# Kernel tuning notes

Measured on AMD Instinct MI355X. Metric: run time of the kernel, lower is better.

## Reference

```python
import jax, jax.numpy as jnp
import numpy as np

# config dims (see shape_source)
NO = 8        # Max_Object
NT = 32       # Max_Time
C = 512       # feat_dims
VD = 1024     # visual_dim
RD = 300      # self.nfeat (relation word-vector dim)
H = 4         # headnum
B = 8         # batch
No = NT * 2 * NO      # 512 object-graph nodes
Nr = NT * NO * NO     # 2048 relation-graph nodes


def _glorot(key, shape):
    fan_in = shape[0]
    return jax.random.normal(key, shape, dtype=jnp.float32) / np.sqrt(fan_in)


def setup_inputs() -> dict:
    key = jax.random.key(0)
    ks = jax.random.split(key, 18)
    inp = {
        "Ao": jax.random.uniform(ks[0], (B, No, No), dtype=jnp.float32),
        "srco": jax.random.normal(ks[1], (B, 1, 1, No, VD), dtype=jnp.float32),
        "Ar": jax.random.uniform(ks[2], (B, Nr, Nr), dtype=jnp.float32),
        "srcr": jax.random.normal(ks[3], (B, 1, 1, Nr, RD), dtype=jnp.float32),
        # GraphConvolution weights: gcl_o/gcl2_o and gcl_r/gcl2_r
        "Wo1": _glorot(ks[4], (VD, 1024)),
        "Wo2": _glorot(ks[5], (1024, C)),
        "Wr1": _glorot(ks[6], (RD, 1024)),
        "Wr2": _glorot(ks[7], (1024, C)),
        # MultiHeadAttention (e2n) projections
        "Wq": _glorot(ks[8], (C, C)), "bq": jnp.zeros((C,), jnp.float32),
        "Wk": _glorot(ks[9], (C, C)), "bk": jnp.zeros((C,), jnp.float32),
        "Wv": _glorot(ks[10], (C, C)), "bv": jnp.zeros((C,), jnp.float32),
        "Wp": _glorot(ks[11], (C, C)), "bp": jnp.zeros((C,), jnp.float32),
        # e2n_embed: Linear(2C -> C)
        "We": _glorot(ks[12], (2 * C, C)), "be": jnp.zeros((C,), jnp.float32),
    }
    return inp


def _gcn2(A, x, W1, W2):
    """Two stacked GraphConvolution layers with self-loops: relu((A+I) @ x @ W).
    A: (b,N,N), x: (b,N,Din). Vectorized over batch (torch code loops per-sample)."""
    eye = jnp.eye(A.shape[-1], dtype=A.dtype)
    Ah = A + eye
    h = jax.nn.relu(jnp.einsum('bij,bjd->bid', Ah, x @ W1))
    return jax.nn.relu(jnp.einsum('bij,bjd->bid', Ah, h @ W2))


def _mha(x, Wq, bq, Wk, bk, Wv, bv, Wp, bp):
    """Standard multi-head self-attention. x: (Bseg, S, C)."""
    Bs, S, _ = x.shape
    dh = C // H
    q = (x @ Wq + bq).reshape(Bs, S, H, dh)
    k = (x @ Wk + bk).reshape(Bs, S, H, dh)
    v = (x @ Wv + bv).reshape(Bs, S, H, dh)
    attn = jax.nn.softmax(jnp.einsum('bqhd,bkhd->bhqk', q, k) / np.sqrt(dh), axis=-1)
    o = jnp.einsum('bhqk,bkhd->bqhd', attn, v).reshape(Bs, S, C)
    return o @ Wp + bp


def _forward(Ao, srco, Ar, srcr, Wo1, Wo2, Wr1, Wr2,
             Wq, bq, Wk, bk, Wv, bv, Wp, bp, We, be):
    b = Ao.shape[0]
    # object-graph GCN (torch loops over batch; vectorized here)
    xo = srco[:, 0, 0, :, :VD]                       # (b, No, VD)
    srco_gcn = _gcn2(Ao, xo, Wo1, Wo2)               # (b, No, C)
    out_gcn_o = srco_gcn.reshape(b, NT, 2 * NO, C)
    # relation-graph GCN
    xr = srcr[:, 0, 0]                               # (b, Nr, RD)
    srcr_gcn = _gcn2(Ar, xr, Wr1, Wr2)               # (b, Nr, C)
    out_gcn_r = srcr_gcn.reshape(b, NT, NO * NO, C)
    # compute_e2n: segment-wise MHA over NO-token windows (torch loops over NO)
    r = out_gcn_r.reshape(b * NT, NO, NO, C)
    seg_a = r.reshape(b * NT * NO, NO, C)                      # rows of NOxNO grid
    a = _mha(seg_a, Wq, bq, Wk, bk, Wv, bv, Wp, bp).mean(axis=1)
    a = a.reshape(b * NT, NO, C)
    seg_o = jnp.swapaxes(r, 1, 2).reshape(b * NT * NO, NO, C)  # cols (permute 0,2,1,3)
    o = _mha(seg_o, Wq, bq, Wk, bk, Wv, bv, Wp, bp).mean(axis=1)
    o = o.reshape(b * NT, NO, C)
    tmp = jnp.concatenate([a, o], axis=1)                      # (b*NT, 2*NO, C)
    cat = jnp.concatenate([tmp, out_gcn_o.reshape(b * NT, 2 * NO, C)], axis=-1)
    out_e2n = cat @ We + be
    return out_e2n.reshape(b, NT, 2 * NO, C)


def reference(Ao, srco, Ar, srcr, Wo1, Wo2, Wr1, Wr2,
              Wq, bq, Wk, bk, Wv, bv, Wp, bp, We, be):
    return _forward(Ao, srco, Ar, srcr, Wo1, Wo2, Wr1, Wr2,
                    Wq, bq, Wk, bk, Wv, bv, Wp, bp, We, be)
```

## Files before the change

kernel.cpp:

```cpp
#include <hip/hip_runtime.h>
#include <hip/hip_bf16.h>


typedef __attribute__((ext_vector_type(4))) float f32x4;
typedef __attribute__((ext_vector_type(8))) short bf16x8s;

#define TILE 128
#define BKK 32
#define LDSS 40

__device__ inline void split2(float a, float b, unsigned& h, unsigned& l) {
    __hip_bfloat16 ha = __float2bfloat16(a), hb = __float2bfloat16(b);
    float ra = __bfloat162float(ha), rb = __bfloat162float(hb);
    __hip_bfloat16 la = __float2bfloat16(a - ra), lb = __float2bfloat16(b - rb);
    unsigned short uha = *(unsigned short*)&ha, uhb = *(unsigned short*)&hb;
    unsigned short ula = *(unsigned short*)&la, ulb = *(unsigned short*)&lb;
    h = (unsigned)uha | ((unsigned)uhb << 16);
    l = (unsigned)ula | ((unsigned)ulb << 16);
}

__global__ __launch_bounds__(256) void gemm_split2(
    const float* __restrict__ A, long long sA, int lda,
    const float* __restrict__ BT, long long sBT, int ldbt,
    float* __restrict__ D, long long sD, int ldd,
    const float* __restrict__ addN, long long sAddN, int ldaddN,
    const float* __restrict__ addT, long long sAddT, int ldaddT,
    const float* __restrict__ bias,
    int K, int relu)
{
    __shared__ __hip_bfloat16 Ah[TILE * LDSS], Al[TILE * LDSS];
    __shared__ __hip_bfloat16 Bh[TILE * LDSS], Bl[TILE * LDSS];

    const int tid  = threadIdx.x;
    const int lane = tid & 63;
    const int wave = tid >> 6;
    const int wm   = (wave >> 1) * 64;
    const int wn   = (wave & 1) * 64;
    const int row0 = blockIdx.y * TILE;
    const int col0 = blockIdx.x * TILE;
    const int b    = blockIdx.z;

    const float* Ab = A  + (size_t)b * sA;
    const float* Bb = BT + (size_t)b * sBT;

    f32x4 acc[4][4];
#pragma unroll
    for (int i = 0; i < 4; ++i)
#pragma unroll
        for (int j = 0; j < 4; ++j) acc[i][j] = (f32x4){0.f, 0.f, 0.f, 0.f};

    const int quad = lane >> 4;
    const int l16  = lane & 15;

    for (int k0 = 0; k0 < K; k0 += BKK) {
        __syncthreads();
#pragma unroll
        for (int it = 0; it < 2; ++it) {
            int task = tid + it * 256;
            int m = task >> 2, kq = task & 3;
            const float* ap = Ab + (size_t)(row0 + m) * lda + k0 + kq * 8;
            float4 v0 = *(const float4*)ap;
            float4 v1 = *(const float4*)(ap + 4);
            uint4 H, L;
            split2(v0.x, v0.y, H.x, L.x); split2(v0.z, v0.w, H.y, L.y);
            split2(v1.x, v1.y, H.z, L.z); split2(v1.z, v1.w, H.w, L.w);
            *(uint4*)(&Ah[m * LDSS + kq * 8]) = H;
            *(uint4*)(&Al[m * LDSS + kq * 8]) = L;
        }
#pragma unroll
        for (int it = 0; it < 2; ++it) {
            int task = tid + it * 256;
            int n = task >> 2, kq = task & 3;
            const float* bp = Bb + (size_t)(col0 + n) * ldbt + k0 + kq * 8;
            float4 v0 = *(const float4*)bp;
            float4 v1 = *(const float4*)(bp + 4);
            uint4 H, L;
            split2(v0.x, v0.y, H.x, L.x); split2(v0.z, v0.w, H.y, L.y);
            split2(v1.x, v1.y, H.z, L.z); split2(v1.z, v1.w, H.w, L.w);
            *(uint4*)(&Bh[n * LDSS + kq * 8]) = H;
            *(uint4*)(&Bl[n * LDSS + kq * 8]) = L;
        }
        __syncthreads();

        bf16x8s ah[4], al[4], bh[4], bl[4];
#pragma unroll
        for (int mt = 0; mt < 4; ++mt) {
            int r = (wm + mt * 16 + l16) * LDSS + quad * 8;
            ah[mt] = *(const bf16x8s*)(&Ah[r]);
            al[mt] = *(const bf16x8s*)(&Al[r]);
        }
#pragma unroll
        for (int nt = 0; nt < 4; ++nt) {
            int r = (wn + nt * 16 + l16) * LDSS + quad * 8;
            bh[nt] = *(const bf16x8s*)(&Bh[r]);
            bl[nt] = *(const bf16x8s*)(&Bl[r]);
        }
#pragma unroll
        for (int mt = 0; mt < 4; ++mt)
#pragma unroll
            for (int nt = 0; nt < 4; ++nt) {
                acc[mt][nt] = __builtin_amdgcn_mfma_f32_16x16x32_bf16(ah[mt], bh[nt], acc[mt][nt], 0, 0, 0);
                acc[mt][nt] = __builtin_amdgcn_mfma_f32_16x16x32_bf16(ah[mt], bl[nt], acc[mt][nt], 0, 0, 0);
                acc[mt][nt] = __builtin_amdgcn_mfma_f32_16x16x32_bf16(al[mt], bh[nt], acc[mt][nt], 0, 0, 0);
            }
    }

    float* Db = D + (size_t)b * sD;
    const float* AddN = addN ? addN + (size_t)b * sAddN : nullptr;
    const float* AddT = addT ? addT + (size_t)b * sAddT : nullptr;
#pragma unroll
    for (int mt = 0; mt < 4; ++mt)
#pragma unroll
        for (int nt = 0; nt < 4; ++nt)
#pragma unroll
            for (int r = 0; r < 4; ++r) {
                int m = row0 + wm + mt * 16 + quad * 4 + r;
                int n = col0 + wn + nt * 16 + l16;
                float v = acc[mt][nt][r];
                if (AddN) v += AddN[(size_t)m * ldaddN + n];
                if (AddT) v += AddT[(size_t)n * ldaddT + m];
                if (bias) v += bias[n];
                if (relu && v < 0.f) v = 0.f;
                Db[(size_t)m * ldd + n] = v;
            }
}

__global__ __launch_bounds__(256) void padtrans(
    const float* __restrict__ src, float* __restrict__ dst,
    int R, int C, int Rp, int Cp)
{
    __shared__ float T[64][65];
    const int t = threadIdx.x;
    const int tr = t >> 4, tc = t & 15;
    const int c0 = blockIdx.x * 64, r0 = blockIdx.y * 64;
    const size_t bat = blockIdx.z;
    const float* sb = src + bat * (size_t)R * C;
    float* db = dst + bat * (size_t)Cp * Rp;

#pragma unroll
    for (int i = 0; i < 4; ++i) {
        int rr = tr + i * 16;
        int gr = r0 + rr;
        float v0 = 0.f, v1 = 0.f, v2 = 0.f, v3 = 0.f;
        if (gr < R) {
            int c = c0 + tc * 4;
            const float* s = sb + (size_t)gr * C + c;
            if (c + 0 < C) v0 = s[0];
            if (c + 1 < C) v1 = s[1];
            if (c + 2 < C) v2 = s[2];
            if (c + 3 < C) v3 = s[3];
        }
        T[rr][tc * 4 + 0] = v0; T[rr][tc * 4 + 1] = v1;
        T[rr][tc * 4 + 2] = v2; T[rr][tc * 4 + 3] = v3;
    }
    __syncthreads();
#pragma unroll
    for (int i = 0; i < 4; ++i) {
        int cc = tr + i * 16;
        float4 v = { T[tc * 4 + 0][cc], T[tc * 4 + 1][cc],
                     T[tc * 4 + 2][cc], T[tc * 4 + 3][cc] };
        *(float4*)(db + (size_t)(c0 + cc) * Rp + r0 + tc * 4) = v;
    }
}

__global__ __launch_bounds__(256) void gemm_bf16(
    const __hip_bfloat16* __restrict__ A, long long sA, int lda,
    const __hip_bfloat16* __restrict__ B, long long sB, int ldb,
    void* __restrict__ D, long long sD, int ldd,
    const __hip_bfloat16* __restrict__ addsrc, long long sAdd, int ldadd,
    const float* __restrict__ bias,
    int K, int relu, int outF32)
{
    __shared__ __hip_bfloat16 As[TILE * LDSS];
    __shared__ __hip_bfloat16 Bs[TILE * LDSS];

    const int tid  = threadIdx.x;
    const int lane = tid & 63;
    const int wave = tid >> 6;
    const int wm   = (wave >> 1) * 64;
    const int wn   = (wave & 1) * 64;
    const int row0 = blockIdx.y * TILE;
    const int col0 = blockIdx.x * TILE;
    const int b    = blockIdx.z;

    const __hip_bfloat16* Ab = A + (size_t)b * sA;
    const __hip_bfloat16* Bb = B + (size_t)b * sB;

    f32x4 acc[4][4];
#pragma unroll
    for (int i = 0; i < 4; ++i)
#pragma unroll
        for (int j = 0; j < 4; ++j) acc[i][j] = (f32x4){0.f, 0.f, 0.f, 0.f};

    const int quad = lane >> 4;
    const int l16  = lane & 15;

    for (int k0 = 0; k0 < K; k0 += BKK) {
        __syncthreads();
#pragma unroll
        for (int it = 0; it < 2; ++it) {
            int task = tid + it * 256;
            int m = task >> 2, kq = task & 3;
            uint4 val = *(const uint4*)(Ab + (size_t)(row0 + m) * lda + k0 + kq * 8);
            *(uint4*)(&As[m * LDSS + kq * 8]) = val;
        }
#pragma unroll
        for (int it = 0; it < 2; ++it) {
            int task = tid + it * 256;
            int kk = task >> 4, n8 = task & 15;
            uint4 val = *(const uint4*)(Bb + (size_t)(k0 + kk) * ldb + col0 + n8 * 8);
            const __hip_bfloat16* v16 = (const __hip_bfloat16*)&val;
#pragma unroll
            for (int u = 0; u < 8; ++u)
                Bs[(n8 * 8 + u) * LDSS + kk] = v16[u];
        }
        __syncthreads();

        bf16x8s afrag[4], bfrag[4];
#pragma unroll
        for (int mt = 0; mt < 4; ++mt)
            afrag[mt] = *(const bf16x8s*)(&As[(wm + mt * 16 + l16) * LDSS + quad * 8]);
#pragma unroll
        for (int nt = 0; nt < 4; ++nt)
            bfrag[nt] = *(const bf16x8s*)(&Bs[(wn + nt * 16 + l16) * LDSS + quad * 8]);
#pragma unroll
        for (int mt = 0; mt < 4; ++mt)
#pragma unroll
            for (int nt = 0; nt < 4; ++nt)
                acc[mt][nt] = __builtin_amdgcn_mfma_f32_16x16x32_bf16(
                    afrag[mt], bfrag[nt], acc[mt][nt], 0, 0, 0);
    }

    __hip_bfloat16* Db16 = (__hip_bfloat16*)D + (size_t)b * sD;
    float*          DbF  = (float*)D + (size_t)b * sD;
    const __hip_bfloat16* Addb = addsrc ? addsrc + (size_t)b * sAdd : nullptr;
#pragma unroll
    for (int mt = 0; mt < 4; ++mt)
#pragma unroll
        for (int nt = 0; nt < 4; ++nt)
#pragma unroll
            for (int r = 0; r < 4; ++r) {
                int m = row0 + wm + mt * 16 + quad * 4 + r;
                int n = col0 + wn + nt * 16 + l16;
                float v = acc[mt][nt][r];
                if (Addb) v += __bfloat162float(Addb[(size_t)m * ldadd + n]);
                if (bias) v += bias[n];
                if (relu && v < 0.f) v = 0.f;
                if (outF32) DbF[(size_t)m * ldd + n] = v;
                else        Db16[(size_t)m * ldd + n] = __float2bfloat16(v);
            }
}

__global__ void convert_kernel(const float* __restrict__ src,
                               __hip_bfloat16* __restrict__ dst, int n4)
{
    int i = blockIdx.x * blockDim.x + threadIdx.x;
    if (i >= n4) return;
    float4 v = ((const float4*)src)[i];
    __hip_bfloat16 t0 = __float2bfloat16(v.x), t1 = __float2bfloat16(v.y);
    __hip_bfloat16 t2 = __float2bfloat16(v.z), t3 = __float2bfloat16(v.w);
    ushort4 o = { *(unsigned short*)&t0, *(unsigned short*)&t1,
                  *(unsigned short*)&t2, *(unsigned short*)&t3 };
    ((ushort4*)dst)[i] = o;
}

__global__ __launch_bounds__(256) void attn_kernel(
    const float* __restrict__ q,
    const float* __restrict__ k,
    const float* __restrict__ v,
    __hip_bfloat16* __restrict__ abar)
{
    __shared__ float qs[8][512], ks[8][512], vs[8][512];
    __shared__ float sc[4][8][8];
    __shared__ float wb[4][8];

    const int tid  = threadIdx.x;
    const int mode = blockIdx.y;
    const int g    = blockIdx.x >> 3;
    const int idx  = blockIdx.x & 7;
    const int rowBase = g * 64;

    for (int t = tid; t < 512; t += 256) {
        int p = t >> 6, c8 = (t & 63) * 8;
        int row = (mode == 0) ? (rowBase + idx * 8 + p) : (rowBase + p * 8 + idx);
        const float* qp = q + (size_t)row * 512 + c8;
        const float* kp = k + (size_t)row * 512 + c8;
        const float* vp = v + (size_t)row * 512 + c8;
        *(float4*)(&qs[p][c8])     = *(const float4*)(qp);
        *(float4*)(&qs[p][c8 + 4]) = *(const float4*)(qp + 4);
        *(float4*)(&ks[p][c8])     = *(const float4*)(kp);
        *(float4*)(&ks[p][c8 + 4]) = *(const float4*)(kp + 4);
        *(float4*)(&vs[p][c8])     = *(const float4*)(vp);
        *(float4*)(&vs[p][c8 + 4]) = *(const float4*)(vp + 4);
    }
    __syncthreads();

    {
        int h = tid >> 6, l = tid & 63;
        int i = l >> 3, j = l & 7;
        const float* qrow = &qs[i][h * 128];
        const float* krow = &ks[j][h * 128];
        float s = 0.f;
#pragma unroll
        for (int d = 0; d < 128; d += 4) {
            float4 qa = *(const float4*)(qrow + d);
            float4 kb = *(const float4*)(krow + d);
            s += qa.x * kb.x + qa.y * kb.y + qa.z * kb.z + qa.w * kb.w;
        }
        sc[h][i][j] = s * 0.08838834764831845f;
    }
    __syncthreads();

    if (tid < 32) {
        int h = tid >> 3, i = tid & 7;
        float mx = -1e30f;
#pragma unroll
        for (int j = 0; j < 8; ++j) mx = fmaxf(mx, sc[h][i][j]);
        float e[8], sum = 0.f;
#pragma unroll
        for (int j = 0; j < 8; ++j) { e[j] = __expf(sc[h][i][j] - mx); sum += e[j]; }
        float inv = 1.f / sum;
#pragma unroll
        for (int j = 0; j < 8; ++j) sc[h][i][j] = e[j] * inv;
    }
    __syncthreads();

    if (tid < 32) {
        int h = tid >> 3, j = tid & 7;
        float s = 0.f;
#pragma unroll
        for (int i = 0; i < 8; ++i) s += sc[h][i][j];
        wb[h][j] = s * 0.125f;
    }
    __syncthreads();

    {
        int orow = g * 16 + mode * 8 + idx;
        for (int c = tid; c < 512; c += 256) {
            int h = c >> 7;
            float o = 0.f;
#pragma unroll
            for (int j = 0; j < 8; ++j) o += wb[h][j] * vs[j][c];
            abar[(size_t)orow * 512 + c] = __float2bfloat16(o);
        }
    }
}


extern "C" void kernel_launch(void* const* d_in, const int* in_sizes, int n_in,
                              void* d_out, int out_size, void* d_ws, size_t ws_size,
                              hipStream_t stream)
{
    const float* Ao   = (const float*)d_in[0];
    const float* srco = (const float*)d_in[1];
    const float* Ar   = (const float*)d_in[2];
    const float* srcr = (const float*)d_in[3];
    const float* Wo1  = (const float*)d_in[4];
    const float* Wo2  = (const float*)d_in[5];
    const float* Wr1  = (const float*)d_in[6];
    const float* Wr2  = (const float*)d_in[7];
    const float* Wq   = (const float*)d_in[8];
    const float* bq   = (const float*)d_in[9];
    const float* Wk   = (const float*)d_in[10];
    const float* bk   = (const float*)d_in[11];
    const float* Wv   = (const float*)d_in[12];
    const float* bv   = (const float*)d_in[13];
    const float* Wp   = (const float*)d_in[14];
    const float* bp   = (const float*)d_in[15];
    const float* We   = (const float*)d_in[16];
    const float* be   = (const float*)d_in[17];
    float* out = (float*)d_out;

    char* ws = (char*)d_ws;
    const size_t R0 = 0;
    const size_t R1 = 67108864;
    const size_t R2 = 100663296;
    const size_t R3 = 134217728;
    const size_t R4 = 167772160;
    const size_t R5 = 192937984;

    float* HRf  = (float*)(ws + R0);
    float* qF   = (float*)(ws + R0);
    float* kF   = (float*)(ws + R0 + 33554432);
    float* T2Rf = (float*)(ws + R1);
    float* vF   = (float*)(ws + R1);
    float* Uf   = (float*)(ws + R2);
    float* T2RT = (float*)(ws + R2);
    float* GRf  = (float*)(ws + R3);
    float* XPT  = (float*)(ws + R4);
    __hip_bfloat16* ABAR = (__hip_bfloat16*)(ws + R4);
    float* WPT  = (float*)(ws + R5);
    float* Wr2T = (float*)(ws + R5 + 1310720);
    float* WqT  = (float*)(ws + R5 + 3407872);
    float* WkT  = (float*)(ws + R5 + 4456448);
    float* WvT  = (float*)(ws + R5 + 5505024);

    __hip_bfloat16* TO    = (__hip_bfloat16*)(ws + R2 + 0);
    __hip_bfloat16* HO    = (__hip_bfloat16*)(ws + R2 + 8388608);
    __hip_bfloat16* T2O   = (__hip_bfloat16*)(ws + R2 + 16777216);
    __hip_bfloat16* CAT   = (__hip_bfloat16*)(ws + R2 + 20971520);
    __hip_bfloat16* srcoB = (__hip_bfloat16*)(ws + R2 + 29360128);
    __hip_bfloat16* AoB   = (__hip_bfloat16*)(ws + R2 + 37748736);
    __hip_bfloat16* Wo1B  = (__hip_bfloat16*)(ws + R2 + 41943040);
    __hip_bfloat16* Wo2B  = (__hip_bfloat16*)(ws + R2 + 44040192);
    __hip_bfloat16* WeB   = (__hip_bfloat16*)(ws + R2 + 45088768);
    __hip_bfloat16* WpB   = (__hip_bfloat16*)(ws + R2 + 46137344);

    dim3 blk(256);
    auto cvt = [&](const float* s, __hip_bfloat16* d, int n) {
        convert_kernel<<<dim3((n / 4 + 255) / 256), blk, 0, stream>>>(s, d, n / 4);
    };

    padtrans<<<dim3(6, 32, 8), blk, 0, stream>>>(srcr, XPT, 2048, 300, 2048, 384);
    padtrans<<<dim3(16, 5, 1), blk, 0, stream>>>(Wr1, WPT, 300, 1024, 320, 1024);
    padtrans<<<dim3(8, 16, 1), blk, 0, stream>>>(Wr2, Wr2T, 1024, 512, 1024, 512);
    padtrans<<<dim3(8, 8, 1), blk, 0, stream>>>(Wq, WqT, 512, 512, 512, 512);
    padtrans<<<dim3(8, 8, 1), blk, 0, stream>>>(Wk, WkT, 512, 512, 512, 512);
    padtrans<<<dim3(8, 8, 1), blk, 0, stream>>>(Wv, WvT, 512, 512, 512, 512);

    gemm_split2<<<dim3(3, 16, 8), blk, 0, stream>>>(
        Ar, 2048LL * 2048, 2048, XPT, 384LL * 2048, 2048,
        Uf, 2048LL * 384, 384, nullptr, 0, 0, XPT, 384LL * 2048, 2048,
        nullptr, 2048, 0);
    gemm_split2<<<dim3(8, 128, 1), blk, 0, stream>>>(
        Uf, 0, 384, WPT, 0, 320,
        HRf, 0, 1024, nullptr, 0, 0, nullptr, 0, 0,
        nullptr, 320, 1);
    gemm_split2<<<dim3(4, 128, 1), blk, 0, stream>>>(
        HRf, 0, 1024, Wr2T, 0, 1024,
        T2Rf, 0, 512, nullptr, 0, 0, nullptr, 0, 0,
        nullptr, 1024, 0);
    padtrans<<<dim3(8, 32, 8), blk, 0, stream>>>(T2Rf, T2RT, 2048, 512, 2048, 512);
    gemm_split2<<<dim3(4, 16, 8), blk, 0, stream>>>(
        Ar, 2048LL * 2048, 2048, T2RT, 512LL * 2048, 2048,
        GRf, 2048LL * 512, 512, T2Rf, 2048LL * 512, 512, nullptr, 0, 0,
        nullptr, 2048, 1);
    gemm_split2<<<dim3(4, 128, 1), blk, 0, stream>>>(
        GRf, 0, 512, WqT, 0, 512, qF, 0, 512,
        nullptr, 0, 0, nullptr, 0, 0, bq, 512, 0);
    gemm_split2<<<dim3(4, 128, 1), blk, 0, stream>>>(
        GRf, 0, 512, WkT, 0, 512, kF, 0, 512,
        nullptr, 0, 0, nullptr, 0, 0, bk, 512, 0);
    gemm_split2<<<dim3(4, 128, 1), blk, 0, stream>>>(
        GRf, 0, 512, WvT, 0, 512, vF, 0, 512,
        nullptr, 0, 0, nullptr, 0, 0, bv, 512, 0);
    attn_kernel<<<dim3(2048, 2), blk, 0, stream>>>(qF, kF, vF, ABAR);

    cvt(srco, srcoB, 4194304);
    cvt(Ao, AoB, 2097152);
    cvt(Wo1, Wo1B, 1048576);
    cvt(Wo2, Wo2B, 524288);
    cvt(We, WeB, 524288);
    cvt(Wp, WpB, 262144);
    gemm_bf16<<<dim3(8, 32, 1), blk, 0, stream>>>(srcoB, 0, 1024, Wo1B, 0, 1024,
        TO, 0, 1024, nullptr, 0, 0, nullptr, 1024, 0, 0);
    gemm_bf16<<<dim3(8, 4, 8), blk, 0, stream>>>(AoB, 512LL * 512, 512, TO, 512LL * 1024, 1024,
        HO, 512LL * 1024, 1024, TO, 512LL * 1024, 1024, nullptr, 512, 1, 0);
    gemm_bf16<<<dim3(4, 32, 1), blk, 0, stream>>>(HO, 0, 1024, Wo2B, 0, 512,
        T2O, 0, 512, nullptr, 0, 0, nullptr, 1024, 0, 0);
    gemm_bf16<<<dim3(4, 4, 8), blk, 0, stream>>>(AoB, 512LL * 512, 512, T2O, 512LL * 512, 512,
        (void*)(CAT + 512), 512LL * 1024, 1024, T2O, 512LL * 512, 512, nullptr, 512, 1, 0);
    gemm_bf16<<<dim3(4, 32, 1), blk, 0, stream>>>(ABAR, 0, 512, WpB, 0, 512,
        CAT, 0, 1024, nullptr, 0, 0, bp, 512, 0, 0);
    gemm_bf16<<<dim3(4, 32, 1), blk, 0, stream>>>(CAT, 0, 1024, WeB, 0, 512,
        out, 0, 512, nullptr, 0, 0, be, 1024, 0, 1);
}
```

Before: 1.200 ms.

## Store intermediates as pre-split bf16 hi/lo planes instead of fp32

The split-bf16 GEMM pipeline now writes its intermediates and transposed weights directly as bf16 high/low planes, so the following GEMMs load them without doing a per-tile fp32-to-bf16 split. This removes repeated split arithmetic inside the GEMM main loops. It also keeps global traffic roughly the same, since two bf16 planes take the same bytes as one fp32. Only the large Ar operand is still split on the fly. Each producer epilogue now does scalar 2-byte stores to two planes, which may be less efficient than before.

```diff
diff --git a/kernel.cpp b/kernel.cpp
--- a/kernel.cpp
+++ b/kernel.cpp
@@ -19,13 +19,22 @@
     l = (unsigned)ula | ((unsigned)ulb << 16);
 }
 
-__global__ __launch_bounds__(256) void gemm_split2(
+__device__ inline void splitw(float v, unsigned short& h, unsigned short& l) {
+    __hip_bfloat16 hb = __float2bfloat16(v);
+    __hip_bfloat16 lb = __float2bfloat16(v - __bfloat162float(hb));
+    h = *(unsigned short*)&hb;
+    l = *(unsigned short*)&lb;
+}
+
+__global__ __launch_bounds__(256) void gemm_asplit(
     const float* __restrict__ A, long long sA, int lda,
-    const float* __restrict__ BT, long long sBT, int ldbt,
-    float* __restrict__ D, long long sD, int ldd,
+    const __hip_bfloat16* __restrict__ BTh, const __hip_bfloat16* __restrict__ BTl,
+    long long sBT, int ldbt,
+    __hip_bfloat16* __restrict__ Dh_, __hip_bfloat16* __restrict__ Dl_,
+    long long sD, int ldd,
     const float* __restrict__ addN, long long sAddN, int ldaddN,
-    const float* __restrict__ addT, long long sAddT, int ldaddT,
-    const float* __restrict__ bias,
+    const __hip_bfloat16* __restrict__ addTh, const __hip_bfloat16* __restrict__ addTl,
+    long long sAddT, int ldaddT,
     int K, int relu)
 {
     __shared__ __hip_bfloat16 Ah[TILE * LDSS], Al[TILE * LDSS];
@@ -40,8 +49,9 @@
     const int col0 = blockIdx.x * TILE;
     const int b    = blockIdx.z;
 
-    const float* Ab = A  + (size_t)b * sA;
-    const float* Bb = BT + (size_t)b * sBT;
+    const float* Ab = A + (size_t)b * sA;
+    const __hip_bfloat16* Bbh = BTh + (size_t)b * sBT;
+    const __hip_bfloat16* Bbl = BTl + (size_t)b * sBT;
 
     f32x4 acc[4][4];
 #pragma unroll
@@ -71,14 +81,9 @@
         for (int it = 0; it < 2; ++it) {
             int task = tid + it * 256;
             int n = task >> 2, kq = task & 3;
-            const float* bp = Bb + (size_t)(col0 + n) * ldbt + k0 + kq * 8;
-            float4 v0 = *(const float4*)bp;
-            float4 v1 = *(const float4*)(bp + 4);
-            uint4 H, L;
-            split2(v0.x, v0.y, H.x, L.x); split2(v0.z, v0.w, H.y, L.y);
-            split2(v1.x, v1.y, H.z, L.z); split2(v1.z, v1.w, H.w, L.w);
-            *(uint4*)(&Bh[n * LDSS + kq * 8]) = H;
-            *(uint4*)(&Bl[n * LDSS + kq * 8]) = L;
+            size_t off = (size_t)(col0 + n) * ldbt + k0 + kq * 8;
+            *(uint4*)(&Bh[n * LDSS + kq * 8]) = *(const uint4*)(Bbh + off);
+            *(uint4*)(&Bl[n * LDSS + kq * 8]) = *(const uint4*)(Bbl + off);
         }
         __syncthreads();
 
@@ -105,9 +110,11 @@
             }
     }
 
-    float* Db = D + (size_t)b * sD;
+    __hip_bfloat16* Dhb = Dh_ + (size_t)b * sD;
+    __hip_bfloat16* Dlb = Dl_ + (size_t)b * sD;
     const float* AddN = addN ? addN + (size_t)b * sAddN : nullptr;
-    const float* AddT = addT ? addT + (size_t)b * sAddT : nullptr;
+    const __hip_bfloat16* ATh = addTh ? addTh + (size_t)b * sAddT : nullptr;
+    const __hip_bfloat16* ATl = addTl ? addTl + (size_t)b * sAddT : nullptr;
 #pragma unroll
     for (int mt = 0; mt < 4; ++mt)
 #pragma unroll
@@ -118,15 +125,124 @@
                 int n = col0 + wn + nt * 16 + l16;
                 float v = acc[mt][nt][r];
                 if (AddN) v += AddN[(size_t)m * ldaddN + n];
-                if (AddT) v += AddT[(size_t)n * ldaddT + m];
+                if (ATh) v += __bfloat162float(ATh[(size_t)n * ldaddT + m])
+                            + __bfloat162float(ATl[(size_t)n * ldaddT + m]);
+                if (relu && v < 0.f) v = 0.f;
+                unsigned short hh, ll;
+                splitw(v, hh, ll);
+                size_t o = (size_t)m * ldd + n;
+                *(unsigned short*)&Dhb[o] = hh;
+                *(unsigned short*)&Dlb[o] = ll;
+            }
+}
+
+__global__ __launch_bounds__(256) void gemm_planes(
+    const __hip_bfloat16* __restrict__ Aph, const __hip_bfloat16* __restrict__ Apl,
+    long long sA, int lda,
+    const __hip_bfloat16* __restrict__ BTh, const __hip_bfloat16* __restrict__ BTl,
+    long long sBT, int ldbt,
+    void* __restrict__ D, __hip_bfloat16* __restrict__ Dl_, long long sD, int ldd,
+    const float* __restrict__ bias,
+    int K, int relu, int outMode)
+{
+    __shared__ __hip_bfloat16 Ah[TILE * LDSS], Al[TILE * LDSS];
+    __shared__ __hip_bfloat16 Bh[TILE * LDSS], Bl[TILE * LDSS];
+
+    const int tid  = threadIdx.x;
+    const int lane = tid & 63;
+    const int wave = tid >> 6;
+    const int wm   = (wave >> 1) * 64;
+    const int wn   = (wave & 1) * 64;
+    const int row0 = blockIdx.y * TILE;
+    const int col0 = blockIdx.x * TILE;
+    const int b    = blockIdx.z;
+
+    const __hip_bfloat16* Abh = Aph + (size_t)b * sA;
+    const __hip_bfloat16* Abl = Apl + (size_t)b * sA;
+    const __hip_bfloat16* Bbh = BTh + (size_t)b * sBT;
+    const __hip_bfloat16* Bbl = BTl + (size_t)b * sBT;
+
+    f32x4 acc[4][4];
+#pragma unroll
+    for (int i = 0; i < 4; ++i)
+#pragma unroll
+        for (int j = 0; j < 4; ++j) acc[i][j] = (f32x4){0.f, 0.f, 0.f, 0.f};
+
+    const int quad = lane >> 4;
+    const int l16  = lane & 15;
+
+    for (int k0 = 0; k0 < K; k0 += BKK) {
+        __syncthreads();
+#pragma unroll
+        for (int it = 0; it < 2; ++it) {
+            int task = tid + it * 256;
+            int m = task >> 2, kq = task & 3;
+            size_t off = (size_t)(row0 + m) * lda + k0 + kq * 8;
+            *(uint4*)(&Ah[m * LDSS + kq * 8]) = *(const uint4*)(Abh + off);
+            *(uint4*)(&Al[m * LDSS + kq * 8]) = *(const uint4*)(Abl + off);
+        }
+#pragma unroll
+        for (int it = 0; it < 2; ++it) {
+            int task = tid + it * 256;
+            int n = task >> 2, kq = task & 3;
+            size_t off = (size_t)(col0 + n) * ldbt + k0 + kq * 8;
+            *(uint4*)(&Bh[n * LDSS + kq * 8]) = *(const uint4*)(Bbh + off);
+            *(uint4*)(&Bl[n * LDSS + kq * 8]) = *(const uint4*)(Bbl + off);
+        }
+        __syncthreads();
+
+        bf16x8s ah[4], al[4], bh[4], bl[4];
+#pragma unroll
+        for (int mt = 0; mt < 4; ++mt) {
+            int r = (wm + mt * 16 + l16) * LDSS + quad * 8;
+            ah[mt] = *(const bf16x8s*)(&Ah[r]);
+            al[mt] = *(const bf16x8s*)(&Al[r]);
+        }
+#pragma unroll
+        for (int nt = 0; nt < 4; ++nt) {
+            int r = (wn + nt * 16 + l16) * LDSS + quad * 8;
+            bh[nt] = *(const bf16x8s*)(&Bh[r]);
+            bl[nt] = *(const bf16x8s*)(&Bl[r]);
+        }
+#pragma unroll
+        for (int mt = 0; mt < 4; ++mt)
+#pragma unroll
+            for (int nt = 0; nt < 4; ++nt) {
+                acc[mt][nt] = __builtin_amdgcn_mfma_f32_16x16x32_bf16(ah[mt], bh[nt], acc[mt][nt], 0, 0, 0);
+                acc[mt][nt] = __builtin_amdgcn_mfma_f32_16x16x32_bf16(ah[mt], bl[nt], acc[mt][nt], 0, 0, 0);
+                acc[mt][nt] = __builtin_amdgcn_mfma_f32_16x16x32_bf16(al[mt], bh[nt], acc[mt][nt], 0, 0, 0);
+            }
+    }
+
+    float* DbF = (float*)D + (size_t)b * sD;
+    __hip_bfloat16* Dhb = (__hip_bfloat16*)D + (size_t)b * sD;
+    __hip_bfloat16* Dlb = Dl_ ? Dl_ + (size_t)b * sD : nullptr;
+#pragma unroll
+    for (int mt = 0; mt < 4; ++mt)
+#pragma unroll
+        for (int nt = 0; nt < 4; ++nt)
+#pragma unroll
+            for (int r = 0; r < 4; ++r) {
+                int m = row0 + wm + mt * 16 + quad * 4 + r;
+                int n = col0 + wn + nt * 16 + l16;
+                float v = acc[mt][nt][r];
                 if (bias) v += bias[n];
                 if (relu && v < 0.f) v = 0.f;
-                Db[(size_t)m * ldd + n] = v;
+                if (outMode == 0) {
+                    DbF[(size_t)m * ldd + n] = v;
+                } else {
+                    unsigned short hh, ll;
+                    splitw(v, hh, ll);
+                    size_t o = (size_t)m * ldd + n;
+                    *(unsigned short*)&Dhb[o] = hh;
+                    *(unsigned short*)&Dlb[o] = ll;
+                }
             }
 }
 
-__global__ __launch_bounds__(256) void padtrans(
-    const float* __restrict__ src, float* __restrict__ dst,
+__global__ __launch_bounds__(256) void padtrans_split(
+    const float* __restrict__ src,
+    __hip_bfloat16* __restrict__ dsth, __hip_bfloat16* __restrict__ dstl,
     int R, int C, int Rp, int Cp)
 {
     __shared__ float T[64][65];
@@ -135,7 +251,8 @@
     const int c0 = blockIdx.x * 64, r0 = blockIdx.y * 64;
     const size_t bat = blockIdx.z;
     const float* sb = src + bat * (size_t)R * C;
-    float* db = dst + bat * (size_t)Cp * Rp;
+    __hip_bfloat16* dhb = dsth + bat * (size_t)Cp * Rp;
+    __hip_bfloat16* dlb = dstl + bat * (size_t)Cp * Rp;
 
 #pragma unroll
     for (int i = 0; i < 4; ++i) {
@@ -159,7 +276,12 @@
         int cc = tr + i * 16;
         float4 v = { T[tc * 4 + 0][cc], T[tc * 4 + 1][cc],
                      T[tc * 4 + 2][cc], T[tc * 4 + 3][cc] };
-        *(float4*)(db + (size_t)(c0 + cc) * Rp + r0 + tc * 4) = v;
+        ushort4 H, L;
+        splitw(v.x, H.x, L.x); splitw(v.y, H.y, L.y);
+        splitw(v.z, H.z, L.z); splitw(v.w, H.w, L.w);
+        size_t off = (size_t)(c0 + cc) * Rp + r0 + tc * 4;
+        *(ushort4*)(dhb + off) = H;
+        *(ushort4*)(dlb + off) = L;
     }
 }
 
@@ -379,21 +501,31 @@
     const size_t R4 = 167772160;
     const size_t R5 = 192937984;
 
-    float* HRf  = (float*)(ws + R0);
+    __hip_bfloat16* HRh = (__hip_bfloat16*)(ws + R0);
+    __hip_bfloat16* HRl = HRh + 16777216;
     float* qF   = (float*)(ws + R0);
     float* kF   = (float*)(ws + R0 + 33554432);
     float* T2Rf = (float*)(ws + R1);
     float* vF   = (float*)(ws + R1);
-    float* Uf   = (float*)(ws + R2);
-    float* T2RT = (float*)(ws + R2);
-    float* GRf  = (float*)(ws + R3);
-    float* XPT  = (float*)(ws + R4);
+    __hip_bfloat16* Uh = (__hip_bfloat16*)(ws + R2);
+    __hip_bfloat16* Ul = Uh + 6291456;
+    __hip_bfloat16* T2RTh = (__hip_bfloat16*)(ws + R2);
+    __hip_bfloat16* T2RTl = T2RTh + 8388608;
+    __hip_bfloat16* GRh = (__hip_bfloat16*)(ws + R3);
+    __hip_bfloat16* GRl = GRh + 8388608;
+    __hip_bfloat16* XPTh = (__hip_bfloat16*)(ws + R4);
+    __hip_bfloat16* XPTl = XPTh + 6291456;
     __hip_bfloat16* ABAR = (__hip_bfloat16*)(ws + R4);
-    float* WPT  = (float*)(ws + R5);
-    float* Wr2T = (float*)(ws + R5 + 1310720);
-    float* WqT  = (float*)(ws + R5 + 3407872);
-    float* WkT  = (float*)(ws + R5 + 4456448);
-    float* WvT  = (float*)(ws + R5 + 5505024);
+    __hip_bfloat16* WPTh = (__hip_bfloat16*)(ws + R5);
+    __hip_bfloat16* WPTl = WPTh + 327680;
+    __hip_bfloat16* Wr2Th = (__hip_bfloat16*)(ws + R5 + 1310720);
+    __hip_bfloat16* Wr2Tl = Wr2Th + 524288;
+    __hip_bfloat16* WqTh = (__hip_bfloat16*)(ws + R5 + 3407872);
+    __hip_bfloat16* WqTl = WqTh + 262144;
+    __hip_bfloat16* WkTh = (__hip_bfloat16*)(ws + R5 + 4456448);
+    __hip_bfloat16* WkTl = WkTh + 262144;
+    __hip_bfloat16* WvTh = (__hip_bfloat16*)(ws + R5 + 5505024);
+    __hip_bfloat16* WvTl = WvTh + 262144;
 
     __hip_bfloat16* TO    = (__hip_bfloat16*)(ws + R2 + 0);
     __hip_bfloat16* HO    = (__hip_bfloat16*)(ws + R2 + 8388608);
@@ -411,39 +543,39 @@
         convert_kernel<<<dim3((n / 4 + 255) / 256), blk, 0, stream>>>(s, d, n / 4);
     };
 
-    padtrans<<<dim3(6, 32, 8), blk, 0, stream>>>(srcr, XPT, 2048, 300, 2048, 384);
-    padtrans<<<dim3(16, 5, 1), blk, 0, stream>>>(Wr1, WPT, 300, 1024, 320, 1024);
-    padtrans<<<dim3(8, 16, 1), blk, 0, stream>>>(Wr2, Wr2T, 1024, 512, 1024, 512);
-    padtrans<<<dim3(8, 8, 1), blk, 0, stream>>>(Wq, WqT, 512, 512, 512, 512);
-    padtrans<<<dim3(8, 8, 1), blk, 0, stream>>>(Wk, WkT, 512, 512, 512, 512);
-    padtrans<<<dim3(8, 8, 1), blk, 0, stream>>>(Wv, WvT, 512, 512, 512, 512);
-
-    gemm_split2<<<dim3(3, 16, 8), blk, 0, stream>>>(
-        Ar, 2048LL * 2048, 2048, XPT, 384LL * 2048, 2048,
-        Uf, 2048LL * 384, 384, nullptr, 0, 0, XPT, 384LL * 2048, 2048,
-        nullptr, 2048, 0);
-    gemm_split2<<<dim3(8, 128, 1), blk, 0, stream>>>(
-        Uf, 0, 384, WPT, 0, 320,
-        HRf, 0, 1024, nullptr, 0, 0, nullptr, 0, 0,
-        nullptr, 320, 1);
-    gemm_split2<<<dim3(4, 128, 1), blk, 0, stream>>>(
-        HRf, 0, 1024, Wr2T, 0, 1024,
-        T2Rf, 0, 512, nullptr, 0, 0, nullptr, 0, 0,
-        nullptr, 1024, 0);
-    padtrans<<<dim3(8, 32, 8), blk, 0, stream>>>(T2Rf, T2RT, 2048, 512, 2048, 512);
-    gemm_split2<<<dim3(4, 16, 8), blk, 0, stream>>>(
-        Ar, 2048LL * 2048, 2048, T2RT, 512LL * 2048, 2048,
-        GRf, 2048LL * 512, 512, T2Rf, 2048LL * 512, 512, nullptr, 0, 0,
-        nullptr, 2048, 1);
-    gemm_split2<<<dim3(4, 128, 1), blk, 0, stream>>>(
-        GRf, 0, 512, WqT, 0, 512, qF, 0, 512,
-        nullptr, 0, 0, nullptr, 0, 0, bq, 512, 0);
-    gemm_split2<<<dim3(4, 128, 1), blk, 0, stream>>>(
-        GRf, 0, 512, WkT, 0, 512, kF, 0, 512,
-        nullptr, 0, 0, nullptr, 0, 0, bk, 512, 0);
-    gemm_split2<<<dim3(4, 128, 1), blk, 0, stream>>>(
-        GRf, 0, 512, WvT, 0, 512, vF, 0, 512,
-        nullptr, 0, 0, nullptr, 0, 0, bv, 512, 0);
+    padtrans_split<<<dim3(6, 32, 8), blk, 0, stream>>>(srcr, XPTh, XPTl, 2048, 300, 2048, 384);
+    padtrans_split<<<dim3(16, 5, 1), blk, 0, stream>>>(Wr1, WPTh, WPTl, 300, 1024, 320, 1024);
+    padtrans_split<<<dim3(8, 16, 1), blk, 0, stream>>>(Wr2, Wr2Th, Wr2Tl, 1024, 512, 1024, 512);
+    padtrans_split<<<dim3(8, 8, 1), blk, 0, stream>>>(Wq, WqTh, WqTl, 512, 512, 512, 512);
+    padtrans_split<<<dim3(8, 8, 1), blk, 0, stream>>>(Wk, WkTh, WkTl, 512, 512, 512, 512);
+    padtrans_split<<<dim3(8, 8, 1), blk, 0, stream>>>(Wv, WvTh, WvTl, 512, 512, 512, 512);
+
+    gemm_asplit<<<dim3(3, 16, 8), blk, 0, stream>>>(
+        Ar, 2048LL * 2048, 2048, XPTh, XPTl, 384LL * 2048, 2048,
+        Uh, Ul, 2048LL * 384, 384,
+        nullptr, 0, 0, XPTh, XPTl, 384LL * 2048, 2048,
+        2048, 0);
+    gemm_planes<<<dim3(8, 128, 1), blk, 0, stream>>>(
+        Uh, Ul, 0, 384, WPTh, WPTl, 0, 320,
+        HRh, HRl, 0, 1024, nullptr, 320, 1, 1);
+    gemm_planes<<<dim3(4, 128, 1), blk, 0, stream>>>(
+        HRh, HRl, 0, 1024, Wr2Th, Wr2Tl, 0, 1024,
+        T2Rf, nullptr, 0, 512, nullptr, 1024, 0, 0);
+    padtrans_split<<<dim3(8, 32, 8), blk, 0, stream>>>(T2Rf, T2RTh, T2RTl, 2048, 512, 2048, 512);
+    gemm_asplit<<<dim3(4, 16, 8), blk, 0, stream>>>(
+        Ar, 2048LL * 2048, 2048, T2RTh, T2RTl, 512LL * 2048, 2048,
+        GRh, GRl, 2048LL * 512, 512,
+        T2Rf, 2048LL * 512, 512, nullptr, nullptr, 0, 0,
+        2048, 1);
+    gemm_planes<<<dim3(4, 128, 1), blk, 0, stream>>>(
+        GRh, GRl, 0, 512, WqTh, WqTl, 0, 512,
+        qF, nullptr, 0, 512, bq, 512, 0, 0);
+    gemm_planes<<<dim3(4, 128, 1), blk, 0, stream>>>(
+        GRh, GRl, 0, 512, WkTh, WkTl, 0, 512,
+        kF, nullptr, 0, 512, bk, 512, 0, 0);
+    gemm_planes<<<dim3(4, 128, 1), blk, 0, stream>>>(
+        GRh, GRl, 0, 512, WvTh, WvTl, 0, 512,
+        vF, nullptr, 0, 512, bv, 512, 0, 0);
     attn_kernel<<<dim3(2048, 2), blk, 0, stream>>>(qF, kF, vF, ABAR);
 
     cvt(srco, srcoB, 4194304);
```

New measurement: 1.203 ms. Within noise of the previous version (+0.2%).
